# Kernel optimization log

Measured on AMD Instinct MI355X. Metric: run time of the kernel, lower is better.

## Reference

```python
import jax, jax.numpy as jnp
import numpy as np

C = 32          # d_model / channels
D_STATE = 32
D_CONV = 4
EXPAND = 2
D_INNER = EXPAND * C          # 64
DT_RANK = (C + 15) // 16      # ceil(32/16) = 2
EPS = 1e-5


def _conv2d(x, w, b):
    # x: (B,C,H,W), w: (O,I,3,3), stride 1, padding 1 (torch Conv2d)
    y = jax.lax.conv_general_dilated(
        x, w, window_strides=(1, 1), padding=[(1, 1), (1, 1)],
        dimension_numbers=("NCHW", "OIHW", "NCHW"))
    return y + b[None, :, None, None]


def _silu(x):
    return x * jax.nn.sigmoid(x)


def _mamba(xs, in_proj_w, conv1d_w, conv1d_b, x_proj_w, dt_proj_w, dt_proj_b,
           A_log, Dp, out_proj_w):
    # xs: (B, L, C)
    xz = xs @ in_proj_w.T                       # (B, L, 2*D_INNER)
    xm, z = jnp.split(xz, 2, axis=-1)           # each (B, L, D_INNER)

    # causal depthwise conv1d along L (torch: padding=d_conv-1 then [..., :L])
    xc = xm.transpose(0, 2, 1)                  # (B, D_INNER, L)
    xc = jax.lax.conv_general_dilated(
        xc, conv1d_w, window_strides=(1,), padding=[(D_CONV - 1, 0)],
        dimension_numbers=("NCH", "OIH", "NCH"),
        feature_group_count=D_INNER)
    xm = _silu((xc + conv1d_b[None, :, None]).transpose(0, 2, 1))  # (B,L,D_INNER)

    x_dbl = xm @ x_proj_w.T                     # (B, L, DT_RANK + 2*D_STATE)
    dt = x_dbl[..., :DT_RANK]
    Bm = x_dbl[..., DT_RANK:DT_RANK + D_STATE]  # (B, L, N)
    Cm = x_dbl[..., DT_RANK + D_STATE:]         # (B, L, N)

    delta = jax.nn.softplus(dt @ dt_proj_w.T + dt_proj_b)  # (B, L, D_INNER)
    A = -jnp.exp(A_log)                                     # (D_INNER, N)

    deltaA = jnp.exp(delta[..., None] * A)                           # (B,L,D,N)
    deltaBx = delta[..., None] * Bm[:, :, None, :] * xm[..., None]   # (B,L,D,N)

    def combine(c1, c2):
        a1, b1 = c1
        a2, b2 = c2
        return a1 * a2, a2 * b1 + b2

    # parallel linear recurrence h_t = deltaA_t * h_{t-1} + deltaBx_t
    _, hstate = jax.lax.associative_scan(combine, (deltaA, deltaBx), axis=1)

    y = jnp.einsum("bldn,bln->bld", hstate, Cm) + xm * Dp
    y = y * _silu(z)
    return y @ out_proj_w.T                     # (B, L, C)


def setup_inputs() -> dict:
    key = jax.random.key(0)
    ks = jax.random.split(key, 16)
    s = 0.02
    inp = {
        "x": jax.random.normal(ks[0], (4, C, 64, 64), dtype=jnp.float32),
        "conv1_w": jax.random.normal(ks[1], (2 * C, C, 3, 3), jnp.float32) * s,
        "conv1_b": jnp.zeros((2 * C,), jnp.float32),
        "conv2_w": jax.random.normal(ks[2], (C, 2 * C, 3, 3), jnp.float32) * s,
        "conv2_b": jnp.zeros((C,), jnp.float32),
        "ln_g": jnp.ones((C,), jnp.float32),
        "ln_b": jnp.zeros((C,), jnp.float32),
        "in_proj_w": jax.random.normal(ks[3], (2 * D_INNER, C), jnp.float32) * s,
        "conv1d_w": jax.random.normal(ks[4], (D_INNER, 1, D_CONV), jnp.float32) * 0.1,
        "conv1d_b": jnp.zeros((D_INNER,), jnp.float32),
        "x_proj_w": jax.random.normal(ks[5], (DT_RANK + 2 * D_STATE, D_INNER), jnp.float32) * s,
        "dt_proj_w": jax.random.normal(ks[6], (D_INNER, DT_RANK), jnp.float32) * 0.1,
        "dt_proj_b": jax.random.normal(ks[7], (D_INNER,), jnp.float32) * 0.1 - 4.0,
        "A_log": jnp.log(jnp.tile(jnp.arange(1, D_STATE + 1, dtype=jnp.float32), (D_INNER, 1))),
        "Dp": jnp.ones((D_INNER,), jnp.float32),
        "out_proj_w": jax.random.normal(ks[8], (C, D_INNER), jnp.float32) * s,
        "smooth_w": jax.random.normal(ks[9], (C, C, 3, 3), jnp.float32) * s,
        "smooth_b": jnp.zeros((C,), jnp.float32),
    }
    return inp


def reference(x, conv1_w, conv1_b, conv2_w, conv2_b, ln_g, ln_b,
              in_proj_w, conv1d_w, conv1d_b, x_proj_w, dt_proj_w, dt_proj_b,
              A_log, Dp, out_proj_w, smooth_w, smooth_b):
    b, c, h, w = x.shape
    # convb residual
    t = jax.nn.relu(_conv2d(x, conv1_w, conv1_b))
    x = _conv2d(t, conv2_w, conv2_b) + x
    # reshape (b,c,h,w) -> (b, h*w, c) row-major (faithful to torch .reshape)
    xs = x.reshape(b, -1, c)
    # LayerNorm over last dim
    mu = jnp.mean(xs, axis=-1, keepdims=True)
    var = jnp.mean(jnp.square(xs - mu), axis=-1, keepdims=True)
    xs = (xs - mu) * jax.lax.rsqrt(var + EPS) * ln_g + ln_b
    # Mamba block
    y = _mamba(xs, in_proj_w, conv1d_w, conv1d_b, x_proj_w, dt_proj_w,
               dt_proj_b, A_log, Dp, out_proj_w)
    y = y.transpose(0, 2, 1).reshape(b, c, h, w)
    return _conv2d(y, smooth_w, smooth_b)
```

## Files before the change

### kernel.cpp

```cpp
#include <hip/hip_runtime.h>
#include <math.h>

#define SEQL 4096
#define L2E 1.44269504088896340736f

#if defined(__has_builtin)
#if __has_builtin(__builtin_amdgcn_exp2f)
#define FAST_EXP2(x) __builtin_amdgcn_exp2f(x)
#endif
#endif
#ifndef FAST_EXP2
#define FAST_EXP2(x) exp2f(x)
#endif

__device__ __forceinline__ float sigmoid_f(float x){ return 1.0f/(1.0f+expf(-x)); }

template<int CI, int CO, int COG, bool RELU, bool RES>
__global__ __launch_bounds__(256) void conv3x3_k(const float* __restrict__ in,
    const float* __restrict__ wgt, const float* __restrict__ bias,
    const float* __restrict__ res, float* __restrict__ out)
{
  constexpr int CIT = CI/4;
  __shared__ float tin[4][2][6][72];
  __shared__ float red[3][4][COG][66];
  const int tid  = threadIdx.x;
  const int lane = tid & 63;
  const int ty   = tid >> 6;
  const int h0   = blockIdx.x * 4;
  const int co0  = blockIdx.y * COG;
  const int b    = blockIdx.z;

  if (lane < 24){
    int cl = lane / 12, rem = lane % 12, r = rem >> 1, side = rem & 1;
    tin[ty][cl][r][side ? 68 : 3] = 0.0f;
  }

  float acc[4][COG];
  #pragma unroll
  for (int rr=0;rr<4;++rr)
    #pragma unroll
    for (int u=0;u<COG;++u) acc[rr][u] = 0.0f;

  const int ci0 = ty*CIT;
  for (int cig = ci0; cig < ci0 + CIT; cig += 2){
    #pragma unroll
    for (int k=0;k<3;++k){
      int idx4 = lane + (k<<6);
      int row  = idx4 >> 4;
      int cl = row/6, r = row - cl*6;
      int w4 = (idx4 & 15) << 2;
      int h  = h0 - 1 + r;
      float4 v = make_float4(0.f,0.f,0.f,0.f);
      if (h>=0 && h<64)
        v = *(const float4*)(in + ((size_t)(b*CI+cig+cl)*64 + h)*64 + w4);
      *(float4*)&tin[ty][cl][r][4+w4] = v;
    }
    #pragma unroll
    for (int cl=0; cl<2; ++cl){
      float rv[6][3];
      #pragma unroll
      for (int r=0;r<6;++r)
        #pragma unroll
        for (int c=0;c<3;++c)
          rv[r][c] = tin[ty][cl][r][3+lane+c];
      #pragma unroll
      for (int u=0;u<COG;++u){
        const float* wp = wgt + ((size_t)(co0+u)*CI + cig + cl)*9;
        #pragma unroll
        for (int rr=0;rr<4;++rr)
          #pragma unroll
          for (int j=0;j<3;++j){
            acc[rr][u] = fmaf(rv[rr+j][0], wp[3*j+0], acc[rr][u]);
            acc[rr][u] = fmaf(rv[rr+j][1], wp[3*j+1], acc[rr][u]);
            acc[rr][u] = fmaf(rv[rr+j][2], wp[3*j+2], acc[rr][u]);
          }
      }
    }
  }
  if (ty > 0){
    #pragma unroll
    for (int rr=0;rr<4;++rr)
      #pragma unroll
      for (int u=0;u<COG;++u) red[ty-1][rr][u][lane] = acc[rr][u];
  }
  __syncthreads();
  if (ty == 0){
    #pragma unroll
    for (int rr=0;rr<4;++rr)
      #pragma unroll
      for (int u=0;u<COG;++u){
        float s = acc[rr][u] + red[0][rr][u][lane] + red[1][rr][u][lane]
                + red[2][rr][u][lane] + bias[co0+u];
        size_t ob = ((size_t)(b*CO+co0+u)*64 + h0+rr)*64 + lane;
        if constexpr (RES)  s += res[ob];
        if constexpr (RELU) s = fmaxf(s, 0.0f);
        out[ob] = s;
      }
  }
}

__global__ __launch_bounds__(512) void mamba_in_k(const float* __restrict__ x2,
    const float* __restrict__ g, const float* __restrict__ be,
    const float* __restrict__ Wip, const float* __restrict__ cw,
    const float* __restrict__ cb, const float* __restrict__ Wxp,
    const float* __restrict__ Wdt, const float* __restrict__ bdt,
    float* __restrict__ xm2, float* __restrict__ szb, float* __restrict__ dlt,
    float* __restrict__ Bm, float* __restrict__ Cm)
{
  __shared__ float xn[68][37];
  __shared__ float xm[64][68];
  __shared__ float xt[64][67];
  __shared__ float xd[64][67];
  const int tid = threadIdx.x, lane = tid & 63, ty = tid >> 6;
  const int bi = blockIdx.x >> 6;
  const int l0 = (blockIdx.x & 63) << 6;

  if (ty < 2){
    int t = ty*64 + lane;
    if (t < 67){
      int tok = l0 - 3 + t;
      if (tok >= 0){
        const float* row = x2 + (size_t)bi*131072 + (size_t)tok*32;
        float v[32];
        #pragma unroll
        for (int c=0;c<32;c+=4){
          float4 f = *(const float4*)(row + c);
          v[c]=f.x; v[c+1]=f.y; v[c+2]=f.z; v[c+3]=f.w;
        }
        float p[8];
        #pragma unroll
        for (int j2=0;j2<8;++j2) p[j2]=v[j2];
        #pragma unroll
        for (int i=8;i<32;i+=8){
          #pragma unroll
          for (int j2=0;j2<8;++j2) p[j2]+=v[i+j2];
        }
        float mu = (((p[0]+p[1])+(p[2]+p[3]))+((p[4]+p[5])+(p[6]+p[7]))) * 0.03125f;
        float q[8];
        #pragma unroll
        for (int j2=0;j2<8;++j2){ float dd=v[j2]-mu; q[j2]=dd*dd; }
        #pragma unroll
        for (int i=8;i<32;i+=8){
          #pragma unroll
          for (int j2=0;j2<8;++j2){ float dd=v[i+j2]-mu; q[j2]+=dd*dd; }
        }
        float var = (((q[0]+q[1])+(q[2]+q[3]))+((q[4]+q[5])+(q[6]+q[7]))) * 0.03125f;
        float rstd = 1.0f / sqrtf(var + 1e-5f);
        #pragma unroll
        for (int c=0;c<32;++c) xn[t][c] = (v[c]-mu)*rstd*g[c] + be[c];
      } else {
        #pragma unroll
        for (int c=0;c<32;++c) xn[t][c] = 0.0f;
      }
    }
  }
  __syncthreads();

  const int d0 = ty*8;
  {
    float xvA[32];
    #pragma unroll
    for (int c=0;c<32;++c) xvA[c] = xn[lane][c];
    #pragma unroll
    for (int jj=0;jj<8;++jj){
      const float* wr = Wip + (d0+jj)*32;
      float a = 0.0f;
      #pragma unroll
      for (int c=0;c<32;++c) a = fmaf(xvA[c], wr[c], a);
      xm[d0+jj][lane] = a;
    }
  }
  if (lane < 3){
    float xvB[32];
    #pragma unroll
    for (int c=0;c<32;++c) xvB[c] = xn[64+lane][c];
    #pragma unroll
    for (int jj=0;jj<8;++jj){
      const float* wr = Wip + (d0+jj)*32;
      float a = 0.0f;
      #pragma unroll
      for (int c=0;c<32;++c) a = fmaf(xvB[c], wr[c], a);
      xm[d0+jj][64+lane] = a;
    }
  }
  {
    float xvC[32];
    #pragma unroll
    for (int c=0;c<32;++c) xvC[c] = xn[lane+3][c];
    #pragma unroll
    for (int jj=0;jj<8;++jj){
      const float* wr = Wip + (64+d0+jj)*32;
      float a = 0.0f;
      #pragma unroll
      for (int c=0;c<32;++c) a = fmaf(xvC[c], wr[c], a);
      szb[((size_t)(bi*64+d0+jj))*SEQL + l0 + lane] = a * sigmoid_f(a);
    }
  }
  __syncthreads();

  #pragma unroll
  for (int jj=0;jj<8;++jj){
    int d = d0 + jj;
    float a = xm[d][lane]*cw[d*4] + xm[d][lane+1]*cw[d*4+1]
            + xm[d][lane+2]*cw[d*4+2] + xm[d][lane+3]*cw[d*4+3] + cb[d];
    float s = a * sigmoid_f(a);
    xt[lane][d] = s;
    xm2[((size_t)(bi*64+d))*SEQL + l0 + lane] = s;
  }
  __syncthreads();

  float xv[64];
  #pragma unroll
  for (int c=0;c<64;++c) xv[c] = xt[lane][c];
  for (int j=ty; j<66; j+=8){
    const float* wr = Wxp + j*64;
    float a = 0.0f;
    #pragma unroll
    for (int c=0;c<64;++c) a = fmaf(xv[c], wr[c], a);
    xd[lane][j] = a;
  }
  __syncthreads();

  float dt0 = xd[lane][0], dt1 = xd[lane][1];
  #pragma unroll
  for (int k=0;k<8;++k){
    int d2 = ty*8 + k;
    float v = dt0*Wdt[d2*2] + dt1*Wdt[d2*2+1] + bdt[d2];
    float sp = fmaxf(v,0.0f) + log1pf(expf(-fabsf(v)));
    dlt[((size_t)(bi*64+d2))*SEQL + l0 + lane] = sp;
  }
  const int which = ty >> 2, gq = ty & 3;
  float* dst = which ? Cm : Bm;
  size_t base = ((size_t)bi*SEQL + l0 + lane)*32 + gq*8;
  const int s0 = 2 + which*32 + gq*8;
  float4 f0, f1;
  f0.x = xd[lane][s0+0]; f0.y = xd[lane][s0+1]; f0.z = xd[lane][s0+2]; f0.w = xd[lane][s0+3];
  f1.x = xd[lane][s0+4]; f1.y = xd[lane][s0+5]; f1.z = xd[lane][s0+6]; f1.w = xd[lane][s0+7];
  *(float4*)(dst + base)     = f0;
  *(float4*)(dst + base + 4) = f1;
}

__global__ __launch_bounds__(256) void scan_p1(const float* __restrict__ dlt,
    const float* __restrict__ xssm, const float* __restrict__ Bm,
    const float* __restrict__ A_log, float* __restrict__ cA, float* __restrict__ cH)
{
  const int tid = threadIdx.x;
  const int n = tid & 31;
  const int chunk = (blockIdx.x & 7)*8 + (tid >> 5);
  const int bd = blockIdx.x >> 3;
  const int b = bd >> 6, d = bd & 63;
  const int l0 = chunk << 6;
  const float Av2 = -expf(A_log[d*32+n]) * L2E;
  const float* del = dlt  + (size_t)bd*SEQL + l0;
  const float* xp  = xssm + (size_t)bd*SEQL + l0;
  const float* Bp  = Bm + ((size_t)b*SEQL + l0)*32 + n;
  float h = 0.0f, aP = 1.0f;
  #pragma unroll 4
  for (int i0=0;i0<64;i0+=4){
    float4 d4 = *(const float4*)(del+i0);
    float4 x4 = *(const float4*)(xp +i0);
    float b0 = Bp[(i0+0)*32], b1 = Bp[(i0+1)*32], b2 = Bp[(i0+2)*32], b3 = Bp[(i0+3)*32];
    float a0 = FAST_EXP2(d4.x*Av2); h = fmaf(a0,h, d4.x*b0*x4.x); aP *= a0;
    float a1 = FAST_EXP2(d4.y*Av2); h = fmaf(a1,h, d4.y*b1*x4.y); aP *= a1;
    float a2 = FAST_EXP2(d4.z*Av2); h = fmaf(a2,h, d4.z*b2*x4.z); aP *= a2;
    float a3 = FAST_EXP2(d4.w*Av2); h = fmaf(a3,h, d4.w*b3*x4.w); aP *= a3;
  }
  int idx = ((bd<<5) + n)*64 + chunk;
  cA[idx] = aP; cH[idx] = h;
}

__global__ __launch_bounds__(128) void scan_comb(const float* __restrict__ cA,
    float* __restrict__ cH)
{
  const int gid = blockIdx.x*128 + threadIdx.x;
  const size_t base = (size_t)gid*64;
  float hrun = 0.0f;
  #pragma unroll 4
  for (int c0=0;c0<64;c0+=4){
    float4 a4 = *(const float4*)(cA + base + c0);
    float4 h4 = *(const float4*)(cH + base + c0);
    float4 o;
    o.x = hrun; hrun = fmaf(a4.x, hrun, h4.x);
    o.y = hrun; hrun = fmaf(a4.y, hrun, h4.y);
    o.z = hrun; hrun = fmaf(a4.z, hrun, h4.z);
    o.w = hrun; hrun = fmaf(a4.w, hrun, h4.w);
    *(float4*)(cH + base + c0) = o;
  }
}

__global__ __launch_bounds__(256) void scan_p2(const float* __restrict__ dlt,
    const float* __restrict__ xssm, const float* __restrict__ Bm,
    const float* __restrict__ Cm, const float* __restrict__ A_log,
    const float* __restrict__ Dp, const float* __restrict__ sz,
    const float* __restrict__ cH, float* __restrict__ yt)
{
  const int tid = threadIdx.x;
  const int n = tid & 31;
  const int chunk = (blockIdx.x & 7)*8 + (tid >> 5);
  const int bd = blockIdx.x >> 3;
  const int b = bd >> 6, d = bd & 63;
  const int l0 = chunk << 6;
  const float Av2 = -expf(A_log[d*32+n]) * L2E;
  const float Dv = Dp[d];
  const float* del = dlt  + (size_t)bd*SEQL + l0;
  const float* xp  = xssm + (size_t)bd*SEQL + l0;
  const float* szp = sz   + (size_t)bd*SEQL + l0;
  const float* Bp  = Bm + ((size_t)b*SEQL + l0)*32 + n;
  const float* Cp  = Cm + ((size_t)b*SEQL + l0)*32 + n;
  float* yp = yt + (size_t)bd*SEQL + l0;
  float h = cH[((bd<<5) + n)*64 + chunk];
  #pragma unroll 2
  for (int i0=0;i0<64;i0+=4){
    float4 d4 = *(const float4*)(del+i0);
    float4 x4 = *(const float4*)(xp +i0);
    float4 s4 = *(const float4*)(szp+i0);
    float b0 = Bp[(i0+0)*32], b1 = Bp[(i0+1)*32], b2 = Bp[(i0+2)*32], b3 = Bp[(i0+3)*32];
    float c0 = Cp[(i0+0)*32], c1 = Cp[(i0+1)*32], c2 = Cp[(i0+2)*32], c3 = Cp[(i0+3)*32];
    float a0 = FAST_EXP2(d4.x*Av2); h = fmaf(a0,h, d4.x*b0*x4.x);
    float v0 = h*c0;
    float a1 = FAST_EXP2(d4.y*Av2); h = fmaf(a1,h, d4.y*b1*x4.y);
    float v1 = h*c1;
    float a2 = FAST_EXP2(d4.z*Av2); h = fmaf(a2,h, d4.z*b2*x4.z);
    float v2 = h*c2;
    float a3 = FAST_EXP2(d4.w*Av2); h = fmaf(a3,h, d4.w*b3*x4.w);
    float v3 = h*c3;
    v0 += __shfl_xor(v0,16); v0 += __shfl_xor(v0,8); v0 += __shfl_xor(v0,4);
    v0 += __shfl_xor(v0,2);  v0 += __shfl_xor(v0,1);
    v1 += __shfl_xor(v1,16); v1 += __shfl_xor(v1,8); v1 += __shfl_xor(v1,4);
    v1 += __shfl_xor(v1,2);  v1 += __shfl_xor(v1,1);
    v2 += __shfl_xor(v2,16); v2 += __shfl_xor(v2,8); v2 += __shfl_xor(v2,4);
    v2 += __shfl_xor(v2,2);  v2 += __shfl_xor(v2,1);
    v3 += __shfl_xor(v3,16); v3 += __shfl_xor(v3,8); v3 += __shfl_xor(v3,4);
    v3 += __shfl_xor(v3,2);  v3 += __shfl_xor(v3,1);
    if (n==0){
      yp[i0+0] = fmaf(x4.x, Dv, v0) * s4.x;
      yp[i0+1] = fmaf(x4.y, Dv, v1) * s4.y;
      yp[i0+2] = fmaf(x4.z, Dv, v2) * s4.z;
      yp[i0+3] = fmaf(x4.w, Dv, v3) * s4.w;
    }
  }
}

__global__ __launch_bounds__(512) void outproj_k(const float* __restrict__ yt,
    const float* __restrict__ Wout, float* __restrict__ ym)
{
  __shared__ float ys[64][67];
  const int tid = threadIdx.x, lane = tid & 63, ty = tid >> 6;
  const int bi = blockIdx.x >> 6;
  const int l0 = (blockIdx.x & 63) << 6;
  for (int r=ty; r<64; r+=8)
    ys[lane][r] = yt[((size_t)(bi*64+r))*SEQL + l0 + lane];
  __syncthreads();
  float yv[64];
  #pragma unroll
  for (int c=0;c<64;++c) yv[c] = ys[lane][c];
  #pragma unroll
  for (int jj=0;jj<4;++jj){
    int j = ty*4 + jj;
    const float* wr = Wout + j*64;
    float acc = 0.0f;
    #pragma unroll
    for (int c=0;c<64;++c) acc = fmaf(yv[c], wr[c], acc);
    ym[((size_t)(bi*32+j))*SEQL + l0 + lane] = acc;
  }
}

extern "C" void kernel_launch(void* const* d_in, const int* in_sizes, int n_in,
                              void* d_out, int out_size, void* d_ws, size_t ws_size,
                              hipStream_t stream) {
  const float* x        = (const float*)d_in[0];
  const float* conv1_w  = (const float*)d_in[1];
  const float* conv1_b  = (const float*)d_in[2];
  const float* conv2_w  = (const float*)d_in[3];
  const float* conv2_b  = (const float*)d_in[4];
  const float* ln_g     = (const float*)d_in[5];
  const float* ln_b     = (const float*)d_in[6];
  const float* in_proj_w= (const float*)d_in[7];
  const float* conv1d_w = (const float*)d_in[8];
  const float* conv1d_b = (const float*)d_in[9];
  const float* x_proj_w = (const float*)d_in[10];
  const float* dt_proj_w= (const float*)d_in[11];
  const float* dt_proj_b= (const float*)d_in[12];
  const float* A_log    = (const float*)d_in[13];
  const float* Dp       = (const float*)d_in[14];
  const float* out_proj_w=(const float*)d_in[15];
  const float* smooth_w = (const float*)d_in[16];
  const float* smooth_b = (const float*)d_in[17];
  float* out = (float*)d_out;

  float* ws = (float*)d_ws;
  float* t      = ws;
  float* x2     = t      + 1048576;
  float* xm2    = x2     + 524288;
  float* szb    = xm2    + 1048576;
  float* dlt    = szb    + 1048576;
  float* Bmat   = dlt    + 1048576;
  float* Cmat   = Bmat   + 524288;
  float* yt     = Cmat   + 524288;
  float* ym     = yt     + 1048576;
  float* cA     = t;
  float* cH     = t + 524288;

  conv3x3_k<32,64,4,true ,false><<<dim3(16,16,4), 256, 0, stream>>>(x,  conv1_w, conv1_b, nullptr, t);
  conv3x3_k<64,32,4,false,true ><<<dim3(16,8,4), 256, 0, stream>>>(t,  conv2_w, conv2_b, x,       x2);
  mamba_in_k  <<<256, 512, 0, stream>>>(x2, ln_g, ln_b, in_proj_w, conv1d_w, conv1d_b,
                                        x_proj_w, dt_proj_w, dt_proj_b,
                                        xm2, szb, dlt, Bmat, Cmat);
  scan_p1     <<<2048, 256, 0, stream>>>(dlt, xm2, Bmat, A_log, cA, cH);
  scan_comb   <<<64,   128, 0, stream>>>(cA, cH);
  scan_p2     <<<2048, 256, 0, stream>>>(dlt, xm2, Bmat, Cmat, A_log, Dp, szb, cH, yt);
  outproj_k   <<<256, 512, 0, stream>>>(yt, out_proj_w, ym);
  conv3x3_k<32,32,4,false,false><<<dim3(16,8,4), 256, 0, stream>>>(ym, smooth_w, smooth_b, nullptr, out);
}
```

Before: 227.8 us.

## Fuse chunk-local scan into input kernel and chunk-combine into scan pass two

Computes per-chunk scan summaries inside mamba_in_k from shared-memory delta, x and B, removing the scan_p1 kernel and its global re-reads. The scan_comb kernel is dropped; each scan_p2 block recomputes the prefix carries for its chunks serially from cA/cH. This saves launches and memory traffic. In exchange it adds serial work at the tail of the input kernel and redundant prefix computation in every p2 block.

```diff
diff --git a/kernel.cpp b/kernel.cpp
--- a/kernel.cpp
+++ b/kernel.cpp
@@ -104,8 +104,10 @@
     const float* __restrict__ Wip, const float* __restrict__ cw,
     const float* __restrict__ cb, const float* __restrict__ Wxp,
     const float* __restrict__ Wdt, const float* __restrict__ bdt,
+    const float* __restrict__ A_log,
     float* __restrict__ xm2, float* __restrict__ szb, float* __restrict__ dlt,
-    float* __restrict__ Bm, float* __restrict__ Cm)
+    float* __restrict__ Bm, float* __restrict__ Cm,
+    float* __restrict__ cA, float* __restrict__ cH)
 {
   __shared__ float xn[68][37];
   __shared__ float xm[64][68];
@@ -209,82 +211,67 @@
   }
   __syncthreads();
 
-  float xv[64];
-  #pragma unroll
-  for (int c=0;c<64;++c) xv[c] = xt[lane][c];
-  for (int j=ty; j<66; j+=8){
-    const float* wr = Wxp + j*64;
-    float a = 0.0f;
-    #pragma unroll
-    for (int c=0;c<64;++c) a = fmaf(xv[c], wr[c], a);
-    xd[lane][j] = a;
-  }
-  __syncthreads();
-
-  float dt0 = xd[lane][0], dt1 = xd[lane][1];
-  #pragma unroll
-  for (int k=0;k<8;++k){
-    int d2 = ty*8 + k;
-    float v = dt0*Wdt[d2*2] + dt1*Wdt[d2*2+1] + bdt[d2];
-    float sp = fmaxf(v,0.0f) + log1pf(expf(-fabsf(v)));
-    dlt[((size_t)(bi*64+d2))*SEQL + l0 + lane] = sp;
-  }
-  const int which = ty >> 2, gq = ty & 3;
-  float* dst = which ? Cm : Bm;
-  size_t base = ((size_t)bi*SEQL + l0 + lane)*32 + gq*8;
-  const int s0 = 2 + which*32 + gq*8;
-  float4 f0, f1;
-  f0.x = xd[lane][s0+0]; f0.y = xd[lane][s0+1]; f0.z = xd[lane][s0+2]; f0.w = xd[lane][s0+3];
-  f1.x = xd[lane][s0+4]; f1.y = xd[lane][s0+5]; f1.z = xd[lane][s0+6]; f1.w = xd[lane][s0+7];
-  *(float4*)(dst + base)     = f0;
-  *(float4*)(dst + base + 4) = f1;
-}
-
-__global__ __launch_bounds__(256) void scan_p1(const float* __restrict__ dlt,
-    const float* __restrict__ xssm, const float* __restrict__ Bm,
-    const float* __restrict__ A_log, float* __restrict__ cA, float* __restrict__ cH)
-{
-  const int tid = threadIdx.x;
-  const int n = tid & 31;
-  const int chunk = (blockIdx.x & 7)*8 + (tid >> 5);
-  const int bd = blockIdx.x >> 3;
-  const int b = bd >> 6, d = bd & 63;
-  const int l0 = chunk << 6;
-  const float Av2 = -expf(A_log[d*32+n]) * L2E;
-  const float* del = dlt  + (size_t)bd*SEQL + l0;
-  const float* xp  = xssm + (size_t)bd*SEQL + l0;
-  const float* Bp  = Bm + ((size_t)b*SEQL + l0)*32 + n;
-  float h = 0.0f, aP = 1.0f;
-  #pragma unroll 4
-  for (int i0=0;i0<64;i0+=4){
-    float4 d4 = *(const float4*)(del+i0);
-    float4 x4 = *(const float4*)(xp +i0);
-    float b0 = Bp[(i0+0)*32], b1 = Bp[(i0+1)*32], b2 = Bp[(i0+2)*32], b3 = Bp[(i0+3)*32];
-    float a0 = FAST_EXP2(d4.x*Av2); h = fmaf(a0,h, d4.x*b0*x4.x); aP *= a0;
-    float a1 = FAST_EXP2(d4.y*Av2); h = fmaf(a1,h, d4.y*b1*x4.y); aP *= a1;
-    float a2 = FAST_EXP2(d4.z*Av2); h = fmaf(a2,h, d4.z*b2*x4.z); aP *= a2;
-    float a3 = FAST_EXP2(d4.w*Av2); h = fmaf(a3,h, d4.w*b3*x4.w); aP *= a3;
-  }
-  int idx = ((bd<<5) + n)*64 + chunk;
-  cA[idx] = aP; cH[idx] = h;
-}
-
-__global__ __launch_bounds__(128) void scan_comb(const float* __restrict__ cA,
-    float* __restrict__ cH)
-{
-  const int gid = blockIdx.x*128 + threadIdx.x;
-  const size_t base = (size_t)gid*64;
-  float hrun = 0.0f;
-  #pragma unroll 4
-  for (int c0=0;c0<64;c0+=4){
-    float4 a4 = *(const float4*)(cA + base + c0);
-    float4 h4 = *(const float4*)(cH + base + c0);
-    float4 o;
-    o.x = hrun; hrun = fmaf(a4.x, hrun, h4.x);
-    o.y = hrun; hrun = fmaf(a4.y, hrun, h4.y);
-    o.z = hrun; hrun = fmaf(a4.z, hrun, h4.z);
-    o.w = hrun; hrun = fmaf(a4.w, hrun, h4.w);
-    *(float4*)(cH + base + c0) = o;
+  {
+    float xv[64];
+    #pragma unroll
+    for (int c=0;c<64;++c) xv[c] = xt[lane][c];
+    for (int j=ty; j<66; j+=8){
+      const float* wr = Wxp + j*64;
+      float a = 0.0f;
+      #pragma unroll
+      for (int c=0;c<64;++c) a = fmaf(xv[c], wr[c], a);
+      xd[lane][j] = a;
+    }
+  }
+  __syncthreads();
+
+  {
+    float dt0 = xd[lane][0], dt1 = xd[lane][1];
+    #pragma unroll
+    for (int k=0;k<8;++k){
+      int d2 = ty*8 + k;
+      float v = dt0*Wdt[d2*2] + dt1*Wdt[d2*2+1] + bdt[d2];
+      float sp = fmaxf(v,0.0f) + log1pf(expf(-fabsf(v)));
+      dlt[((size_t)(bi*64+d2))*SEQL + l0 + lane] = sp;
+      xm[d2][lane] = sp;
+    }
+    const int which = ty >> 2, gq = ty & 3;
+    float* dst = which ? Cm : Bm;
+    size_t base = ((size_t)bi*SEQL + l0 + lane)*32 + gq*8;
+    const int s0 = 2 + which*32 + gq*8;
+    float4 f0, f1;
+    f0.x = xd[lane][s0+0]; f0.y = xd[lane][s0+1]; f0.z = xd[lane][s0+2]; f0.w = xd[lane][s0+3];
+    f1.x = xd[lane][s0+4]; f1.y = xd[lane][s0+5]; f1.z = xd[lane][s0+6]; f1.w = xd[lane][s0+7];
+    *(float4*)(dst + base)     = f0;
+    *(float4*)(dst + base + 4) = f1;
+  }
+  __syncthreads();
+
+  {
+    const int d  = tid >> 3;
+    const int gg = tid & 7;
+    const int chunk = blockIdx.x & 63;
+    const int bd = bi*64 + d;
+    float Av2[4], h[4] = {0,0,0,0}, aP[4] = {1,1,1,1};
+    #pragma unroll
+    for (int j=0;j<4;++j) Av2[j] = -expf(A_log[d*32 + gg + 8*j]) * L2E;
+    #pragma unroll 4
+    for (int t=0;t<64;++t){
+      float dlv = xm[d][t];
+      float xv2 = xt[t][d];
+      #pragma unroll
+      for (int j=0;j<4;++j){
+        float bv = xd[t][2 + gg + 8*j];
+        float a = FAST_EXP2(dlv*Av2[j]);
+        h[j] = fmaf(a, h[j], dlv*bv*xv2);
+        aP[j] *= a;
+      }
+    }
+    #pragma unroll
+    for (int j=0;j<4;++j){
+      size_t idx = (((size_t)bd<<5) + gg + 8*j)*64 + chunk;
+      cA[idx] = aP[j]; cH[idx] = h[j];
+    }
   }
 }
 
@@ -292,14 +279,46 @@
     const float* __restrict__ xssm, const float* __restrict__ Bm,
     const float* __restrict__ Cm, const float* __restrict__ A_log,
     const float* __restrict__ Dp, const float* __restrict__ sz,
-    const float* __restrict__ cH, float* __restrict__ yt)
+    const float* __restrict__ cA, const float* __restrict__ cHs,
+    float* __restrict__ yt)
 {
+  __shared__ float pre[32][9];
   const int tid = threadIdx.x;
   const int n = tid & 31;
-  const int chunk = (blockIdx.x & 7)*8 + (tid >> 5);
+  const int grp = blockIdx.x & 7;
+  const int chunk = grp*8 + (tid >> 5);
   const int bd = blockIdx.x >> 3;
   const int b = bd >> 6, d = bd & 63;
   const int l0 = chunk << 6;
+
+  if (tid < 32){
+    const float* pa = cA  + (((size_t)bd<<5)+tid)*64;
+    const float* ph = cHs + (((size_t)bd<<5)+tid)*64;
+    float hrun = 0.0f;
+    for (int c=0;c<grp*8;c+=4){
+      float4 a4 = *(const float4*)(pa+c);
+      float4 h4 = *(const float4*)(ph+c);
+      hrun = fmaf(a4.x,hrun,h4.x);
+      hrun = fmaf(a4.y,hrun,h4.y);
+      hrun = fmaf(a4.z,hrun,h4.z);
+      hrun = fmaf(a4.w,hrun,h4.w);
+    }
+    int c = grp*8;
+    float4 a4 = *(const float4*)(pa+c);
+    float4 h4 = *(const float4*)(ph+c);
+    pre[tid][0]=hrun; hrun=fmaf(a4.x,hrun,h4.x);
+    pre[tid][1]=hrun; hrun=fmaf(a4.y,hrun,h4.y);
+    pre[tid][2]=hrun; hrun=fmaf(a4.z,hrun,h4.z);
+    pre[tid][3]=hrun; hrun=fmaf(a4.w,hrun,h4.w);
+    a4 = *(const float4*)(pa+c+4);
+    h4 = *(const float4*)(ph+c+4);
+    pre[tid][4]=hrun; hrun=fmaf(a4.x,hrun,h4.x);
+    pre[tid][5]=hrun; hrun=fmaf(a4.y,hrun,h4.y);
+    pre[tid][6]=hrun; hrun=fmaf(a4.z,hrun,h4.z);
+    pre[tid][7]=hrun;
+  }
+  __syncthreads();
+
   const float Av2 = -expf(A_log[d*32+n]) * L2E;
   const float Dv = Dp[d];
   const float* del = dlt  + (size_t)bd*SEQL + l0;
@@ -308,7 +327,7 @@
   const float* Bp  = Bm + ((size_t)b*SEQL + l0)*32 + n;
   const float* Cp  = Cm + ((size_t)b*SEQL + l0)*32 + n;
   float* yp = yt + (size_t)bd*SEQL + l0;
-  float h = cH[((bd<<5) + n)*64 + chunk];
+  float h = pre[n][tid >> 5];
   #pragma unroll 2
   for (int i0=0;i0<64;i0+=4){
     float4 d4 = *(const float4*)(del+i0);
@@ -404,11 +423,9 @@
   conv3x3_k<32,64,4,true ,false><<<dim3(16,16,4), 256, 0, stream>>>(x,  conv1_w, conv1_b, nullptr, t);
   conv3x3_k<64,32,4,false,true ><<<dim3(16,8,4), 256, 0, stream>>>(t,  conv2_w, conv2_b, x,       x2);
   mamba_in_k  <<<256, 512, 0, stream>>>(x2, ln_g, ln_b, in_proj_w, conv1d_w, conv1d_b,
-                                        x_proj_w, dt_proj_w, dt_proj_b,
-                                        xm2, szb, dlt, Bmat, Cmat);
-  scan_p1     <<<2048, 256, 0, stream>>>(dlt, xm2, Bmat, A_log, cA, cH);
-  scan_comb   <<<64,   128, 0, stream>>>(cA, cH);
-  scan_p2     <<<2048, 256, 0, stream>>>(dlt, xm2, Bmat, Cmat, A_log, Dp, szb, cH, yt);
+                                        x_proj_w, dt_proj_w, dt_proj_b, A_log,
+                                        xm2, szb, dlt, Bmat, Cmat, cA, cH);
+  scan_p2     <<<2048, 256, 0, stream>>>(dlt, xm2, Bmat, Cmat, A_log, Dp, szb, cA, cH, yt);
   outproj_k   <<<256, 512, 0, stream>>>(yt, out_proj_w, ym);
   conv3x3_k<32,32,4,false,false><<<dim3(16,8,4), 256, 0, stream>>>(ym, smooth_w, smooth_b, nullptr, out);
 }
```

New measurement: 223.0 us. -2.1%, faster.
